# Kernel tuning notes

Measured on AMD Instinct MI355X. Metric: run time of the kernel, lower is better.

## Reference

```python
import jax, jax.numpy as jnp
import numpy as np
from jax.ops import segment_sum

N = 50000
E = 1600000
B = 1000  # number of graphs
F_IN, H, OUT = 64, 128, 10


def setup_inputs() -> dict:
    key = jax.random.key(0)
    ks = jax.random.split(key, 16)
    x = jax.random.normal(ks[0], (N, F_IN), dtype=jnp.float32)
    edge_index = jax.random.randint(ks[1], (2, E), 0, N, dtype=jnp.int64)
    batch = jnp.sort(jax.random.randint(ks[2], (N,), 0, B, dtype=jnp.int64))

    def glorot(k, fan_in, fan_out):
        s = jnp.sqrt(6.0 / (fan_in + fan_out))
        return jax.random.uniform(k, (fan_in, fan_out), jnp.float32, -s, s)

    return {
        "x": x, "edge_index": edge_index, "batch": batch,
        "W1": glorot(ks[3], F_IN, H), "b1": jnp.zeros((H,), jnp.float32),
        "W2": glorot(ks[4], H, H), "b2": jnp.zeros((H,), jnp.float32),
        "W3": glorot(ks[5], H, H // 2), "b3": jnp.zeros((H // 2,), jnp.float32),
        "Wl1": glorot(ks[6], H // 2, H // 4), "bl1": jnp.zeros((H // 4,), jnp.float32),
        "Wl2": glorot(ks[7], H // 4, OUT), "bl2": jnp.zeros((OUT,), jnp.float32),
    }


def _gcn_conv(x, src, dst, dinv, W, b):
    # GCNConv: h = x W; out_i = sum_{j->i} dinv_j * dinv_i * h_j ; + bias
    h = x @ W
    norm = dinv[src] * dinv[dst]                      # [E+N]
    msg = h[src] * norm[:, None]                      # gather + scale
    out = segment_sum(msg, dst, num_segments=N)       # scatter-add
    return out + b


def reference(x, edge_index, batch, W1, b1, W2, b2, W3, b3, Wl1, bl1, Wl2, bl2):
    # add self-loops (static shape E+N)
    loops = jnp.arange(N, dtype=edge_index.dtype)
    src = jnp.concatenate([edge_index[0], loops])
    dst = jnp.concatenate([edge_index[1], loops])
    # symmetric degree normalization from target degrees (incl. self-loops)
    deg = segment_sum(jnp.ones_like(dst, dtype=x.dtype), dst, num_segments=N)
    dinv = jnp.where(deg > 0, jax.lax.rsqrt(jnp.maximum(deg, 1.0)), 0.0)

    h = jax.nn.relu(_gcn_conv(x, src, dst, dinv, W1, b1))   # dropout: eval mode (identity)
    h = jax.nn.relu(_gcn_conv(h, src, dst, dinv, W2, b2))
    h = jax.nn.relu(_gcn_conv(h, src, dst, dinv, W3, b3))

    # global mean pool over graphs
    sums = segment_sum(h, batch, num_segments=B)            # [B, H//2]
    cnts = segment_sum(jnp.ones((N,), h.dtype), batch, num_segments=B)
    g = sums / jnp.maximum(cnts, 1.0)[:, None]

    g = jax.nn.relu(g @ Wl1 + bl1)
    return g @ Wl2 + bl2
```

## Files before the change

### kernel.cpp

```cpp
#include <hip/hip_runtime.h>
#include <hip/hip_bf16.h>
#include <hip/hip_fp16.h>

#define CHUNK 8192
#define WN    128
#define NBMAX 512

typedef _Float16 f16x8 __attribute__((ext_vector_type(8)));
typedef float    f32x4 __attribute__((ext_vector_type(4)));


__global__ __launch_bounds__(256) void k_rhist(const int* __restrict__ dst, int* __restrict__ H,
                                               int E, int NC, int NB) {
    __shared__ int h[NBMAX];
    int c = blockIdx.x, t = threadIdx.x;
    for (int i = t; i < NB; i += 256) h[i] = 0;
    __syncthreads();
    int base = c * CHUNK;
    int lim = min(CHUNK, E - base);
    for (int k = t; k < lim; k += 256) atomicAdd(&h[dst[base + k] >> 7], 1);
    __syncthreads();
    for (int i = t; i < NB; i += 256) H[i * NC + c] = h[i];
}

__global__ __launch_bounds__(256) void k_scanA(const int* __restrict__ in, int* __restrict__ out,
                                               int* __restrict__ bsum, int n) {
    __shared__ int s[256];
    int i = blockIdx.x * 256 + threadIdx.x;
    int v = (i < n) ? in[i] : 0;
    s[threadIdx.x] = v;
    __syncthreads();
    for (int off = 1; off < 256; off <<= 1) {
        int x = (threadIdx.x >= off) ? s[threadIdx.x - off] : 0;
        __syncthreads();
        s[threadIdx.x] += x;
        __syncthreads();
    }
    if (i < n) out[i] = s[threadIdx.x] - v;
    if (threadIdx.x == 255) bsum[blockIdx.x] = s[255];
}

__global__ __launch_bounds__(512) void k_scanB(int* __restrict__ bsum, int nb) {
    __shared__ int s[512];
    int t = threadIdx.x;
    int v = (t < nb) ? bsum[t] : 0;
    s[t] = v;
    __syncthreads();
    for (int off = 1; off < 512; off <<= 1) {
        int x = (t >= off) ? s[t - off] : 0;
        __syncthreads();
        s[t] += x;
        __syncthreads();
    }
    if (t < nb) bsum[t] = s[t] - v;
}

__global__ __launch_bounds__(256) void k_scanC(int* __restrict__ out, const int* __restrict__ bsum,
                                               int n) {
    int i = blockIdx.x * 256 + threadIdx.x;
    if (i < n) out[i] += bsum[blockIdx.x];
}

__global__ __launch_bounds__(256) void k_rscatter(const int* __restrict__ src, const int* __restrict__ dst,
                                                  const int* __restrict__ O, int* __restrict__ packed,
                                                  int E, int NC, int NB) {
    __shared__ int cur[NBMAX];
    int c = blockIdx.x, t = threadIdx.x;
    for (int i = t; i < NB; i += 256) cur[i] = O[i * NC + c];
    __syncthreads();
    int base = c * CHUNK;
    int lim = min(CHUNK, E - base);
    for (int k = t; k < lim; k += 256) {
        int d = dst[base + k];
        int p = atomicAdd(&cur[d >> 7], 1);
        packed[p] = (src[base + k] << 7) | (d & (WN - 1));
    }
}

__global__ __launch_bounds__(256) void k_wincsr(const int* __restrict__ packed,
                                                const int* __restrict__ O,
                                                int* __restrict__ row_start,
                                                int* __restrict__ csr,
                                                float* __restrict__ dinv,
                                                int n, int NC, int NB, int E) {
    __shared__ int cnt[WN];
    __shared__ int ss[256];
    __shared__ int cur[WN];
    int b = blockIdx.x, t = threadIdx.x;
    int s = O[b * NC];
    int e = (b + 1 < NB) ? O[(b + 1) * NC] : E;
    if (t < WN) cnt[t] = 0;
    __syncthreads();
    for (int k = s + t; k < e; k += 256) atomicAdd(&cnt[packed[k] & (WN - 1)], 1);
    __syncthreads();
    int v = (t < WN) ? cnt[t] : 0;
    ss[t] = v;
    __syncthreads();
    for (int off = 1; off < WN; off <<= 1) {
        int x = (t >= off) ? ss[t - off] : 0;
        __syncthreads();
        ss[t] += x;
        __syncthreads();
    }
    int node = b * WN + t;
    if (t < WN) {
        int start = s + ss[t] - v;
        cur[t] = start;
        if (node < n) {
            row_start[node] = start;
            dinv[node] = rsqrtf((float)(cnt[t] + 1));
        }
    }
    if (b == NB - 1 && t == 0) row_start[n] = E;
    __syncthreads();
    for (int k = s + t; k < e; k += 256) {
        int r = packed[k];
        int p = atomicAdd(&cur[r & (WN - 1)], 1);
        csr[p] = r >> 7;
    }
}


__global__ __launch_bounds__(256) void k_w2h(const float* __restrict__ W, _Float16* __restrict__ Wt,
                                             int K, int F) {
    int idx = blockIdx.x * 256 + threadIdx.x;
    if (idx < K * F) {
        int k = idx / F, f = idx % F;
        Wt[f * K + k] = (_Float16)W[idx];
    }
}


__global__ __launch_bounds__(256) void k_prescale(const float* __restrict__ x,
                                                  const float* __restrict__ dinv,
                                                  __half* __restrict__ y, int n) {
    int idx = blockIdx.x * 256 + threadIdx.x;
    if (idx >= n * 16) return;
    int i = idx >> 4;
    float dv = dinv[i];
    float4 v = ((const float4*)x)[idx];
    __half2 h0 = __floats2half2_rn(v.x * dv, v.y * dv);
    __half2 h1 = __floats2half2_rn(v.z * dv, v.w * dv);
    uint2 u;
    u.x = *(unsigned int*)&h0;
    u.y = *(unsigned int*)&h1;
    ((uint2*)y)[idx] = u;
}


template <int K, int F, int EPI>
__global__ __launch_bounds__(256) void k_gemm_mfma(const __half* __restrict__ X,
                                                   const _Float16* __restrict__ Wt,
                                                   const float* __restrict__ dinv,
                                                   const float* __restrict__ bias,
                                                   __half* __restrict__ H, int n) {
    constexpr int ROWS = 64;
    constexpr int XS   = K + 8;
    __shared__ _Float16 sX[ROWS * XS];
    __shared__ _Float16 sW[F * XS];
    int row0 = blockIdx.x * ROWS;
    int t = threadIdx.x;

    const uint4* Xg = (const uint4*)X;
    for (int i = t; i < ROWS * (K / 8); i += 256) {
        int r = i / (K / 8), k8 = i % (K / 8);
        int gr = row0 + r;
        uint4 v = (gr < n) ? Xg[(size_t)gr * (K / 8) + k8] : make_uint4(0, 0, 0, 0);
        *(uint4*)&sX[r * XS + k8 * 8] = v;
    }
    const uint4* Wg = (const uint4*)Wt;
    for (int i = t; i < F * (K / 8); i += 256) {
        int f = i / (K / 8), k8 = i % (K / 8);
        *(uint4*)&sW[f * XS + k8 * 8] = Wg[i];
    }
    __syncthreads();

    int w = t >> 6, l = t & 63;
    int wrow = w * 16;
    int lr = l & 15;
    int lk = (l >> 4) * 8;
    f32x4 acc[F / 16];
#pragma unroll
    for (int c = 0; c < F / 16; ++c) acc[c] = (f32x4){0.f, 0.f, 0.f, 0.f};

#pragma unroll
    for (int kb = 0; kb < K / 32; ++kb) {
        f16x8 a = *(const f16x8*)&sX[(wrow + lr) * XS + kb * 32 + lk];
#pragma unroll
        for (int c = 0; c < F / 16; ++c) {
            f16x8 b = *(const f16x8*)&sW[(c * 16 + lr) * XS + kb * 32 + lk];
            acc[c] = __builtin_amdgcn_mfma_f32_16x16x32_f16(a, b, acc[c], 0, 0, 0);
        }
    }

    int rbase = row0 + wrow + (l >> 4) * 4;
    if (EPI == 0) {
        float dv[4];
#pragma unroll
        for (int r = 0; r < 4; ++r) dv[r] = (rbase + r < n) ? dinv[rbase + r] : 0.f;
#pragma unroll
        for (int c = 0; c < F / 16; ++c) {
            int col = c * 16 + lr;
#pragma unroll
            for (int r = 0; r < 4; ++r) {
                int gr = rbase + r;
                if (gr < n) H[(size_t)gr * F + col] = __float2half(acc[c][r] * dv[r]);
            }
        }
    } else {
#pragma unroll
        for (int c = 0; c < F / 16; ++c) {
            int col = c * 16 + lr;
            float bc = bias[col];
#pragma unroll
            for (int r = 0; r < 4; ++r) {
                int gr = rbase + r;
                if (gr < n) H[(size_t)gr * F + col] = __float2half(fmaxf(acc[c][r] + bc, 0.f));
            }
        }
    }
}


__device__ __forceinline__ void acc8(float* a, uint4 v) {
    const __half2* h = (const __half2*)&v;
#pragma unroll
    for (int i = 0; i < 4; ++i) {
        float2 f = __half22float2(h[i]);
        a[2 * i]     += f.x;
        a[2 * i + 1] += f.y;
    }
}

template <int F, int EPI>
__global__ void k_agg_h(const __half* __restrict__ HN, const int* __restrict__ csr,
                        const int* __restrict__ rs, const float* __restrict__ dinv,
                        const float* __restrict__ bias, __half* __restrict__ OUT, int n) {
    constexpr int LPN = F / 8;
    constexpr int NPB = 256 / LPN;
    int node = blockIdx.x * NPB + threadIdx.x / LPN;
    int l    = threadIdx.x % LPN;
    if (node >= n) return;
    const uint4* hn = (const uint4*)HN;
    size_t base = (size_t)node * LPN + l;
    float a[8];
    {
        uint4 v = hn[base];
        const __half2* h = (const __half2*)&v;
#pragma unroll
        for (int i = 0; i < 4; ++i) {
            float2 f = __half22float2(h[i]);
            a[2 * i] = f.x; a[2 * i + 1] = f.y;
        }
    }
    int s = rs[node], e = rs[node + 1];
    int k = s;
    for (; k + 4 <= e; k += 4) {
        int s0 = csr[k], s1 = csr[k + 1], s2 = csr[k + 2], s3 = csr[k + 3];
        uint4 v0 = hn[(size_t)s0 * LPN + l];
        uint4 v1 = hn[(size_t)s1 * LPN + l];
        uint4 v2 = hn[(size_t)s2 * LPN + l];
        uint4 v3 = hn[(size_t)s3 * LPN + l];
        acc8(a, v0); acc8(a, v1); acc8(a, v2); acc8(a, v3);
    }
    for (; k < e; ++k) acc8(a, hn[(size_t)csr[k] * LPN + l]);

    float dv = dinv[node];
    float o[8];
    if (EPI == 0) {
#pragma unroll
        for (int j = 0; j < 8; ++j) o[j] = a[j] * dv;
    } else {
        const float4* b4 = (const float4*)bias;
        float4 bb0 = b4[l * 2], bb1 = b4[l * 2 + 1];
        o[0] = fmaxf(fmaf(a[0], dv, bb0.x), 0.f);
        o[1] = fmaxf(fmaf(a[1], dv, bb0.y), 0.f);
        o[2] = fmaxf(fmaf(a[2], dv, bb0.z), 0.f);
        o[3] = fmaxf(fmaf(a[3], dv, bb0.w), 0.f);
        o[4] = fmaxf(fmaf(a[4], dv, bb1.x), 0.f);
        o[5] = fmaxf(fmaf(a[5], dv, bb1.y), 0.f);
        o[6] = fmaxf(fmaf(a[6], dv, bb1.z), 0.f);
        o[7] = fmaxf(fmaf(a[7], dv, bb1.w), 0.f);
    }
    uint4 u;
    __half2 p0 = __floats2half2_rn(o[0], o[1]);
    __half2 p1 = __floats2half2_rn(o[2], o[3]);
    __half2 p2 = __floats2half2_rn(o[4], o[5]);
    __half2 p3 = __floats2half2_rn(o[6], o[7]);
    u.x = *(unsigned int*)&p0; u.y = *(unsigned int*)&p1;
    u.z = *(unsigned int*)&p2; u.w = *(unsigned int*)&p3;
    ((uint4*)OUT)[base] = u;
}


__global__ void k_gstart(const int* __restrict__ batch, int* __restrict__ gstart,
                         int n, int B) {
    int i = blockIdx.x * 256 + threadIdx.x;
    if (i >= n) return;
    int b = batch[i];
    if (i == 0) {
        for (int g = 0; g <= b; ++g) gstart[g] = 0;
    } else {
        int prev = batch[i - 1];
        if (prev != b)
            for (int g = prev + 1; g <= b; ++g) gstart[g] = i;
    }
    if (i == n - 1)
        for (int g = b + 1; g <= B; ++g) gstart[g] = n;
}

__global__ void k_poolhead(const __half* __restrict__ H3, const int* __restrict__ gstart,
                           const float* __restrict__ Wl1, const float* __restrict__ bl1,
                           const float* __restrict__ Wl2, const float* __restrict__ bl2,
                           float* __restrict__ out, int B) {
    __shared__ float sh[4][64];
    __shared__ float shid[4][32];
    int w = threadIdx.x >> 6;
    int lane = threadIdx.x & 63;
    int g = blockIdx.x * 4 + w;
    if (g < B) {
        int s = gstart[g], e = gstart[g + 1];
        float acc = 0.f;
        for (int i = s; i < e; ++i) acc += __half2float(H3[(size_t)i * 64 + lane]);
        float cnt = fmaxf((float)(e - s), 1.f);
        sh[w][lane] = acc / cnt;
    }
    __syncthreads();
    if (g < B && lane < 32) {
        float a = bl1[lane];
        for (int k = 0; k < 64; ++k) a = fmaf(sh[w][k], Wl1[k * 32 + lane], a);
        shid[w][lane] = fmaxf(a, 0.f);
    }
    __syncthreads();
    if (g < B && lane < 10) {
        float a = bl2[lane];
        for (int k = 0; k < 32; ++k) a = fmaf(shid[w][k], Wl2[k * 10 + lane], a);
        out[g * 10 + lane] = a;
    }
}


extern "C" void kernel_launch(void* const* d_in, const int* in_sizes, int n_in,
                              void* d_out, int out_size, void* d_ws, size_t ws_size,
                              hipStream_t stream) {
    const float* x    = (const float*)d_in[0];
    const int*   ei   = (const int*)d_in[1];
    const int*   batch= (const int*)d_in[2];
    const float* W1   = (const float*)d_in[3];
    const float* b1   = (const float*)d_in[4];
    const float* W2   = (const float*)d_in[5];
    const float* b2   = (const float*)d_in[6];
    const float* W3   = (const float*)d_in[7];
    const float* b3   = (const float*)d_in[8];
    const float* Wl1  = (const float*)d_in[9];
    const float* bl1  = (const float*)d_in[10];
    const float* Wl2  = (const float*)d_in[11];
    const float* bl2  = (const float*)d_in[12];

    const int N  = in_sizes[0] / 64;
    const int E  = in_sizes[1] / 2;
    const int B  = out_size / 10;
    const int NB = (N + WN - 1) / WN;
    const int NC = (E + CHUNK - 1) / CHUNK;
    const int NBNC = NB * NC;
    const int GS = (NBNC + 255) / 256;
    const int* srcI = ei;
    const int* dstI = ei + E;

    char* p = (char*)d_ws;
    auto alloc = [&](size_t bytes) {
        char* r = p;
        p += (bytes + 255) & ~(size_t)255;
        return r;
    };
    int*   H        = (int*)alloc((size_t)NBNC * 4);
    int*   O        = (int*)alloc((size_t)NBNC * 4);
    int*   bsum     = (int*)alloc(2048 * 4);
    int*   packed   = (int*)alloc((size_t)E * 4);
    int*   csr      = (int*)alloc((size_t)E * 4);
    int*   row_start= (int*)alloc((size_t)(N + 1) * 4);
    float* dinv     = (float*)alloc((size_t)N * 4);
    int*   gstart   = (int*)alloc((size_t)(B + 1) * 4);
    _Float16* W1t   = (_Float16*)alloc((size_t)64 * 128 * 2);
    _Float16* W2t   = (_Float16*)alloc((size_t)128 * 128 * 2);
    _Float16* W3t   = (_Float16*)alloc((size_t)128 * 64 * 2);
    __half* bufA    = (__half*)alloc((size_t)N * 128 * 2);
    __half* bufB    = (__half*)alloc((size_t)N * 128 * 2);

    int gN = (N + 255) / 256;

    k_rhist   <<<NC, 256, 0, stream>>>(dstI, H, E, NC, NB);
    k_scanA   <<<GS, 256, 0, stream>>>(H, O, bsum, NBNC);
    k_scanB   <<<1, 512, 0, stream>>>(bsum, GS);
    k_scanC   <<<GS, 256, 0, stream>>>(O, bsum, NBNC);
    k_rscatter<<<NC, 256, 0, stream>>>(srcI, dstI, O, packed, E, NC, NB);
    k_wincsr  <<<NB, 256, 0, stream>>>(packed, O, row_start, csr, dinv, N, NC, NB, E);

    k_w2h<<<(64 * 128 + 255) / 256, 256, 0, stream>>>(W1, W1t, 64, 128);
    k_w2h<<<(128 * 128 + 255) / 256, 256, 0, stream>>>(W2, W2t, 128, 128);
    k_w2h<<<(128 * 64 + 255) / 256, 256, 0, stream>>>(W3, W3t, 128, 64);

    int gG = (N + 63) / 64;
    k_prescale<<<(N * 16 + 255) / 256, 256, 0, stream>>>(x, dinv, bufA, N);
    k_agg_h<64, 0><<<(N + 31) / 32, 256, 0, stream>>>(bufA, csr, row_start, dinv,
                                                      dinv, bufB, N);
    k_gemm_mfma<64, 128, 1><<<gG, 256, 0, stream>>>(bufB, W1t, dinv, b1, bufA, N);
    k_gemm_mfma<128, 128, 0><<<gG, 256, 0, stream>>>(bufA, W2t, dinv, b2, bufB, N);
    k_agg_h<128, 1><<<(N + 15) / 16, 256, 0, stream>>>(bufB, csr, row_start, dinv,
                                                       b2, bufA, N);
    k_gemm_mfma<128, 64, 0><<<gG, 256, 0, stream>>>(bufA, W3t, dinv, b3, bufB, N);
    k_agg_h<64, 1><<<(N + 31) / 32, 256, 0, stream>>>(bufB, csr, row_start, dinv,
                                                      b3, bufA, N);

    k_gstart  <<<gN, 256, 0, stream>>>(batch, gstart, N, B);
    k_poolhead<<<(B + 3) / 4, 256, 0, stream>>>(bufA, gstart, Wl1, bl1, Wl2, bl2,
                                                (float*)d_out, B);
}
```

Measured before the change: 234.3 us.

## Split 128-wide aggregation into two 64-wide column passes and fuse prescale

The layer-2 GEMM now writes its output as two separate 64-column half buffers, and aggregation runs as two 64-feature passes that write interleaved into the 128-wide output. The aim is a smaller gathered working set per pass (N×64 halves), so random neighbor gathers hit L2/MALL more often. The input prescale is fused into the CSR-building kernel, and the three weight conversions are merged into one launch, removing launches and a pass over dinv. The cost is reading the CSR and row starts twice, and adding more work to the CSR kernel's tail.

Result: faster. 223.0 us (-4.8%).

```diff
diff --git a/kernel.cpp b/kernel.cpp
--- a/kernel.cpp
+++ b/kernel.cpp
@@ -82,10 +82,13 @@
                                                 int* __restrict__ row_start,
                                                 int* __restrict__ csr,
                                                 float* __restrict__ dinv,
+                                                const float* __restrict__ x,
+                                                __half* __restrict__ y,
                                                 int n, int NC, int NB, int E) {
     __shared__ int cnt[WN];
     __shared__ int ss[256];
     __shared__ int cur[WN];
+    __shared__ float sdv[WN];
     int b = blockIdx.x, t = threadIdx.x;
     int s = O[b * NC];
     int e = (b + 1 < NB) ? O[(b + 1) * NC] : E;
@@ -97,18 +100,20 @@
     ss[t] = v;
     __syncthreads();
     for (int off = 1; off < WN; off <<= 1) {
-        int x = (t >= off) ? ss[t - off] : 0;
-        __syncthreads();
-        ss[t] += x;
+        int x2 = (t >= off) ? ss[t - off] : 0;
+        __syncthreads();
+        ss[t] += x2;
         __syncthreads();
     }
     int node = b * WN + t;
     if (t < WN) {
         int start = s + ss[t] - v;
         cur[t] = start;
+        float dv = rsqrtf((float)(cnt[t] + 1));
+        sdv[t] = dv;
         if (node < n) {
             row_start[node] = start;
-            dinv[node] = rsqrtf((float)(cnt[t] + 1));
+            dinv[node] = dv;
         }
     }
     if (b == NB - 1 && t == 0) row_start[n] = E;
@@ -118,42 +123,50 @@
         int p = atomicAdd(&cur[r & (WN - 1)], 1);
         csr[p] = r >> 7;
     }
-}
-
-
-__global__ __launch_bounds__(256) void k_w2h(const float* __restrict__ W, _Float16* __restrict__ Wt,
-                                             int K, int F) {
+    int node0 = b * WN;
+    for (int i = t; i < WN * 16; i += 256) {
+        int nd = i >> 4, c4 = i & 15;
+        int g = node0 + nd;
+        if (g < n) {
+            float dv = sdv[nd];
+            float4 vv = ((const float4*)x)[(size_t)g * 16 + c4];
+            __half2 h0 = __floats2half2_rn(vv.x * dv, vv.y * dv);
+            __half2 h1 = __floats2half2_rn(vv.z * dv, vv.w * dv);
+            uint2 u;
+            u.x = *(unsigned int*)&h0;
+            u.y = *(unsigned int*)&h1;
+            ((uint2*)y)[(size_t)g * 16 + c4] = u;
+        }
+    }
+}
+
+
+__global__ __launch_bounds__(256) void k_w2h3(const float* __restrict__ W1, _Float16* __restrict__ W1t,
+                                              const float* __restrict__ W2, _Float16* __restrict__ W2t,
+                                              const float* __restrict__ W3, _Float16* __restrict__ W3t) {
     int idx = blockIdx.x * 256 + threadIdx.x;
-    if (idx < K * F) {
-        int k = idx / F, f = idx % F;
-        Wt[f * K + k] = (_Float16)W[idx];
-    }
-}
-
-
-__global__ __launch_bounds__(256) void k_prescale(const float* __restrict__ x,
-                                                  const float* __restrict__ dinv,
-                                                  __half* __restrict__ y, int n) {
-    int idx = blockIdx.x * 256 + threadIdx.x;
-    if (idx >= n * 16) return;
-    int i = idx >> 4;
-    float dv = dinv[i];
-    float4 v = ((const float4*)x)[idx];
-    __half2 h0 = __floats2half2_rn(v.x * dv, v.y * dv);
-    __half2 h1 = __floats2half2_rn(v.z * dv, v.w * dv);
-    uint2 u;
-    u.x = *(unsigned int*)&h0;
-    u.y = *(unsigned int*)&h1;
-    ((uint2*)y)[idx] = u;
-}
-
-
-template <int K, int F, int EPI>
+    if (idx < 8192) {
+        int k = idx >> 7, f = idx & 127;
+        W1t[f * 64 + k] = (_Float16)W1[idx];
+    } else if (idx < 24576) {
+        int i = idx - 8192;
+        int k = i >> 7, f = i & 127;
+        W2t[f * 128 + k] = (_Float16)W2[i];
+    } else if (idx < 32768) {
+        int i = idx - 24576;
+        int k = i >> 6, f = i & 63;
+        W3t[f * 128 + k] = (_Float16)W3[i];
+    }
+}
+
+
+template <int K, int F, int EPI, bool SP>
 __global__ __launch_bounds__(256) void k_gemm_mfma(const __half* __restrict__ X,
                                                    const _Float16* __restrict__ Wt,
                                                    const float* __restrict__ dinv,
                                                    const float* __restrict__ bias,
-                                                   __half* __restrict__ H, int n) {
+                                                   __half* __restrict__ Hl,
+                                                   __half* __restrict__ Hh, int n) {
     constexpr int ROWS = 64;
     constexpr int XS   = K + 8;
     __shared__ _Float16 sX[ROWS * XS];
@@ -204,7 +217,15 @@
 #pragma unroll
             for (int r = 0; r < 4; ++r) {
                 int gr = rbase + r;
-                if (gr < n) H[(size_t)gr * F + col] = __float2half(acc[c][r] * dv[r]);
+                if (gr < n) {
+                    __half hv = __float2half(acc[c][r] * dv[r]);
+                    if (SP) {
+                        if (c < F / 32) Hl[(size_t)gr * (F / 2) + col] = hv;
+                        else            Hh[(size_t)gr * (F / 2) + col - F / 2] = hv;
+                    } else {
+                        Hl[(size_t)gr * F + col] = hv;
+                    }
+                }
             }
         }
     } else {
@@ -215,7 +236,15 @@
 #pragma unroll
             for (int r = 0; r < 4; ++r) {
                 int gr = rbase + r;
-                if (gr < n) H[(size_t)gr * F + col] = __float2half(fmaxf(acc[c][r] + bc, 0.f));
+                if (gr < n) {
+                    __half hv = __float2half(fmaxf(acc[c][r] + bc, 0.f));
+                    if (SP) {
+                        if (c < F / 32) Hl[(size_t)gr * (F / 2) + col] = hv;
+                        else            Hh[(size_t)gr * (F / 2) + col - F / 2] = hv;
+                    } else {
+                        Hl[(size_t)gr * F + col] = hv;
+                    }
+                }
             }
         }
     }
@@ -235,7 +264,8 @@
 template <int F, int EPI>
 __global__ void k_agg_h(const __half* __restrict__ HN, const int* __restrict__ csr,
                         const int* __restrict__ rs, const float* __restrict__ dinv,
-                        const float* __restrict__ bias, __half* __restrict__ OUT, int n) {
+                        const float* __restrict__ bias, __half* __restrict__ OUT,
+                        int n, int ostride4, int ooff4) {
     constexpr int LPN = F / 8;
     constexpr int NPB = 256 / LPN;
     int node = blockIdx.x * NPB + threadIdx.x / LPN;
@@ -289,7 +319,7 @@
     __half2 p3 = __floats2half2_rn(o[6], o[7]);
     u.x = *(unsigned int*)&p0; u.y = *(unsigned int*)&p1;
     u.z = *(unsigned int*)&p2; u.w = *(unsigned int*)&p3;
-    ((uint4*)OUT)[base] = u;
+    ((uint4*)OUT)[(size_t)node * ostride4 + ooff4 + l] = u;
 }
 
 
@@ -386,33 +416,37 @@
     _Float16* W3t   = (_Float16*)alloc((size_t)128 * 64 * 2);
     __half* bufA    = (__half*)alloc((size_t)N * 128 * 2);
     __half* bufB    = (__half*)alloc((size_t)N * 128 * 2);
+    __half* bufB2   = bufB + (size_t)N * 64;
 
     int gN = (N + 255) / 256;
+    int gG = (N + 63) / 64;
 
     k_rhist   <<<NC, 256, 0, stream>>>(dstI, H, E, NC, NB);
     k_scanA   <<<GS, 256, 0, stream>>>(H, O, bsum, NBNC);
     k_scanB   <<<1, 512, 0, stream>>>(bsum, GS);
     k_scanC   <<<GS, 256, 0, stream>>>(O, bsum, NBNC);
     k_rscatter<<<NC, 256, 0, stream>>>(srcI, dstI, O, packed, E, NC, NB);
-    k_wincsr  <<<NB, 256, 0, stream>>>(packed, O, row_start, csr, dinv, N, NC, NB, E);
-
-    k_w2h<<<(64 * 128 + 255) / 256, 256, 0, stream>>>(W1, W1t, 64, 128);
-    k_w2h<<<(128 * 128 + 255) / 256, 256, 0, stream>>>(W2, W2t, 128, 128);
-    k_w2h<<<(128 * 64 + 255) / 256, 256, 0, stream>>>(W3, W3t, 128, 64);
-
-    int gG = (N + 63) / 64;
-    k_prescale<<<(N * 16 + 255) / 256, 256, 0, stream>>>(x, dinv, bufA, N);
+    k_wincsr  <<<NB, 256, 0, stream>>>(packed, O, row_start, csr, dinv, x, bufA,
+                                       N, NC, NB, E);
+
+    k_w2h3<<<128, 256, 0, stream>>>(W1, W1t, W2, W2t, W3, W3t);
+
     k_agg_h<64, 0><<<(N + 31) / 32, 256, 0, stream>>>(bufA, csr, row_start, dinv,
-                                                      dinv, bufB, N);
-    k_gemm_mfma<64, 128, 1><<<gG, 256, 0, stream>>>(bufB, W1t, dinv, b1, bufA, N);
-    k_gemm_mfma<128, 128, 0><<<gG, 256, 0, stream>>>(bufA, W2t, dinv, b2, bufB, N);
-    k_agg_h<128, 1><<<(N + 15) / 16, 256, 0, stream>>>(bufB, csr, row_start, dinv,
-                                                       b2, bufA, N);
-    k_gemm_mfma<128, 64, 0><<<gG, 256, 0, stream>>>(bufA, W3t, dinv, b3, bufB, N);
+                                                      dinv, bufB, N, 8, 0);
+    k_gemm_mfma<64, 128, 1, false><<<gG, 256, 0, stream>>>(bufB, W1t, dinv, b1,
+                                                           bufA, nullptr, N);
+    k_gemm_mfma<128, 128, 0, true><<<gG, 256, 0, stream>>>(bufA, W2t, dinv, b2,
+                                                           bufB, bufB2, N);
+    k_agg_h<64, 1><<<(N + 31) / 32, 256, 0, stream>>>(bufB,  csr, row_start, dinv,
+                                                      b2,      bufA, N, 16, 0);
+    k_agg_h<64, 1><<<(N + 31) / 32, 256, 0, stream>>>(bufB2, csr, row_start, dinv,
+                                                      b2 + 64, bufA, N, 16, 8);
+    k_gemm_mfma<128, 64, 0, false><<<gG, 256, 0, stream>>>(bufA, W3t, dinv, b3,
+                                                           bufB, nullptr, N);
     k_agg_h<64, 1><<<(N + 31) / 32, 256, 0, stream>>>(bufB, csr, row_start, dinv,
-                                                      b3, bufA, N);
+                                                      b3, bufB2, N, 8, 0);
 
     k_gstart  <<<gN, 256, 0, stream>>>(batch, gstart, N, B);
-    k_poolhead<<<(B + 3) / 4, 256, 0, stream>>>(bufA, gstart, Wl1, bl1, Wl2, bl2,
+    k_poolhead<<<(B + 3) / 4, 256, 0, stream>>>(bufB2, gstart, Wl1, bl1, Wl2, bl2,
                                                 (float*)d_out, B);
 }
```
